# Performance work log

Hardware: AMD Instinct MI355X
Metric: run time of the kernel (lower is better)

The kernel has to match this reference:

```python
import jax, jax.numpy as jnp
import numpy as np

ALPHA = 1.0

def setup_inputs() -> dict:
    key = jax.random.key(0)
    k1, k2, k3, k4 = jax.random.split(key, 4)
    B, N, D = 2048, 32768, 128
    return {
        "anchor": jax.random.normal(k1, (B, D), dtype=jnp.float32),
        "positive": jax.random.normal(k2, (B, D), dtype=jnp.float32),
        "negative": jax.random.normal(k3, (N, D), dtype=jnp.float32),
        "r_score": jax.random.normal(k4, (B, 1), dtype=jnp.float32),
    }

def reference(anchor, positive, negative, r_score):
    # pos_sim: [B,1] elementwise dot per row
    pos_sim = jnp.sum(anchor * positive, axis=1, keepdims=True)
    # neg_mul: [B,N] score matrix; row-wise stable logsumexp -> [B,1]
    neg_mul = jnp.matmul(anchor, negative.T)
    neg_sim = jax.scipy.special.logsumexp(neg_mul, axis=1, keepdims=True)
    loss = jax.nn.relu(neg_sim - pos_sim + r_score + ALPHA)
    return jnp.mean(loss)
```

## Files before the change

kernel.cpp:

```cpp
#include <hip/hip_runtime.h>
#include <hip/hip_bf16.h>


#define B_ROWS 2048
#define N_NEG  32768
#define DIM    128
#define LOG2E  1.4426950408889634f
#define LN2    0.6931471805599453f

typedef __bf16 bf16x8 __attribute__((ext_vector_type(8)));
typedef float  f32x4  __attribute__((ext_vector_type(4)));

static __device__ inline unsigned short f2bf(float f) {
    union { float f; unsigned u; } v; v.f = f;
    unsigned r = v.u + 0x7FFF + ((v.u >> 16) & 1);
    return (unsigned short)(r >> 16);
}

static __device__ inline void load_lds16(const void* g, void* s) {
    __builtin_amdgcn_global_load_lds(
        (const __attribute__((address_space(1))) void*)g,
        (__attribute__((address_space(3))) void*)s,
        16, 0, 0);
}

__global__ void prep(const float* __restrict__ anchor,
                     const float* __restrict__ positive,
                     const float* __restrict__ neg,
                     unsigned short* __restrict__ a_bf,
                     unsigned short* __restrict__ n_bf,
                     float* __restrict__ pos_sim,
                     float* __restrict__ sumexp) {
    int t = threadIdx.x;
    if (blockIdx.x < 256) {
        int row = blockIdx.x * 8 + (t >> 5);
        int c4  = (t & 31) * 4;
        const float4 a4 = *(const float4*)(anchor   + row * DIM + c4);
        const float4 p4 = *(const float4*)(positive + row * DIM + c4);
        float dot = a4.x * p4.x + a4.y * p4.y + a4.z * p4.z + a4.w * p4.w;
        ushort4 ab;
        ab.x = f2bf(a4.x * LOG2E); ab.y = f2bf(a4.y * LOG2E);
        ab.z = f2bf(a4.z * LOG2E); ab.w = f2bf(a4.w * LOG2E);
        *(ushort4*)(a_bf + row * DIM + c4) = ab;
        #pragma unroll
        for (int m = 1; m <= 16; m <<= 1) dot += __shfl_xor(dot, m, 64);
        if ((t & 31) == 0) { pos_sim[row] = dot; sumexp[row] = 0.0f; }
    } else {
        int i = (blockIdx.x - 256) * 256 + t;
        #pragma unroll
        for (int k = 0; k < 4; k++) {
            int idx = i + k * (1024 * 256);
            float4 v = *(const float4*)(neg + (size_t)idx * 4);
            ushort4 o;
            o.x = f2bf(v.x); o.y = f2bf(v.y); o.z = f2bf(v.z); o.w = f2bf(v.w);
            *(ushort4*)(n_bf + (size_t)idx * 4) = o;
        }
    }
}

#define CHUNK 1024
#define TSTEPS (CHUNK / 128)

__global__ __launch_bounds__(256, 2) void fused_gemm_lse(
        const unsigned short* __restrict__ A,
        const unsigned short* __restrict__ Nb,
        float* __restrict__ sumexp) {
    __shared__ unsigned short lds[2][128 * 128];

    const int bid     = blockIdx.x;
    const int rowTile = bid & 15;
    const int chunk   = bid >> 4;
    const int wave = threadIdx.x >> 6, lane = threadIdx.x & 63;
    const int wr = wave >> 1, wc = wave & 1;
    const int q = lane >> 4, c = lane & 15;
    const int lrow = lane >> 4;
    const int lchk = lane & 15;

    const unsigned short* Ag = A + rowTile * (128 * DIM);
    const unsigned short* Bg = Nb + (size_t)(chunk * CHUNK) * DIM;

    #pragma unroll
    for (int i = 0; i < 8; i++) {
        int off = wave * 4096 + i * 512;
        int r   = (off >> 7) + lrow;
        int gofs = r * DIM + ((lchk ^ (r & 7)) << 3);
        load_lds16(Ag + gofs, &lds[0][off]);
        load_lds16(Bg + gofs, &lds[1][off]);
    }
    asm volatile("s_waitcnt vmcnt(0)" ::: "memory");
    __syncthreads();

    int swz[4];
    #pragma unroll
    for (int k = 0; k < 4; k++) swz[k] = (((k * 4 + q) ^ (c & 7)) << 3);

    bf16x8 af[4][4];
    #pragma unroll
    for (int i = 0; i < 4; i++) {
        int row = wr * 64 + i * 16 + c;
        #pragma unroll
        for (int k = 0; k < 4; k++)
            af[i][k] = *(const bf16x8*)&lds[0][row * DIM + swz[k]];
    }
    __syncthreads();

    const f32x4 zero4 = {0.f, 0.f, 0.f, 0.f};
    f32x4 sumacc[4] = {zero4, zero4, zero4, zero4};

    for (int t = 0; t < TSTEPS; t++) {
        const int cur = 1 - (t & 1);
        const int nxt = t & 1;
        if (t + 1 < TSTEPS) {
            const unsigned short* Bn = Bg + (size_t)(t + 1) * 128 * DIM;
            #pragma unroll
            for (int i = 0; i < 8; i++) {
                int off = wave * 4096 + i * 512;
                int r   = (off >> 7) + lrow;
                int gofs = r * DIM + ((lchk ^ (r & 7)) << 3);
                load_lds16(Bn + gofs, &lds[nxt][off]);
            }
        }
        #pragma unroll
        for (int j = 0; j < 4; j++) {
            int brow = wc * 64 + j * 16 + c;
            bf16x8 bf[4];
            #pragma unroll
            for (int k = 0; k < 4; k++)
                bf[k] = *(const bf16x8*)&lds[cur][brow * DIM + swz[k]];
            #pragma unroll
            for (int i = 0; i < 4; i++) {
                f32x4 acc = __builtin_amdgcn_mfma_f32_16x16x32_bf16(af[i][0], bf[0], zero4, 0, 0, 0);
                acc = __builtin_amdgcn_mfma_f32_16x16x32_bf16(af[i][1], bf[1], acc, 0, 0, 0);
                acc = __builtin_amdgcn_mfma_f32_16x16x32_bf16(af[i][2], bf[2], acc, 0, 0, 0);
                acc = __builtin_amdgcn_mfma_f32_16x16x32_bf16(af[i][3], bf[3], acc, 0, 0, 0);
                sumacc[i][0] += __builtin_amdgcn_exp2f(acc[0]);
                sumacc[i][1] += __builtin_amdgcn_exp2f(acc[1]);
                sumacc[i][2] += __builtin_amdgcn_exp2f(acc[2]);
                sumacc[i][3] += __builtin_amdgcn_exp2f(acc[3]);
            }
        }
        if (t + 1 < TSTEPS) {
            asm volatile("s_waitcnt vmcnt(0)" ::: "memory");
            __syncthreads();
        }
    }

    #pragma unroll
    for (int i = 0; i < 4; i++) {
        #pragma unroll
        for (int r = 0; r < 4; r++) {
            float v = sumacc[i][r];
            v += __shfl_xor(v, 1, 64);
            v += __shfl_xor(v, 2, 64);
            v += __shfl_xor(v, 4, 64);
            v += __shfl_xor(v, 8, 64);
            if ((lane & 15) == 0) {
                int row = rowTile * 128 + wr * 64 + i * 16 + q * 4 + r;
                atomicAdd(&sumexp[row], v);
            }
        }
    }
}

__global__ void finalize(const float* __restrict__ sumexp,
                         const float* __restrict__ pos_sim,
                         const float* __restrict__ r_score,
                         float* __restrict__ out) {
    __shared__ float red[4];
    int t = threadIdx.x;
    float acc = 0.0f;
    #pragma unroll
    for (int i = 0; i < 8; i++) {
        int row = t + i * 256;
        float lse  = __log2f(sumexp[row]) * LN2;
        float loss = lse - pos_sim[row] + r_score[row] + 1.0f;
        acc += fmaxf(loss, 0.0f);
    }
    #pragma unroll
    for (int m = 1; m <= 32; m <<= 1) acc += __shfl_xor(acc, m, 64);
    if ((t & 63) == 0) red[t >> 6] = acc;
    __syncthreads();
    if (t == 0) out[0] = (red[0] + red[1] + red[2] + red[3]) * (1.0f / (float)B_ROWS);
}

extern "C" void kernel_launch(void* const* d_in, const int* in_sizes, int n_in,
                              void* d_out, int out_size, void* d_ws, size_t ws_size,
                              hipStream_t stream) {
    const float* anchor   = (const float*)d_in[0];
    const float* positive = (const float*)d_in[1];
    const float* negative = (const float*)d_in[2];
    const float* r_score  = (const float*)d_in[3];
    float* out = (float*)d_out;

    char* ws = (char*)d_ws;
    float* sumexp           = (float*)ws;
    float* pos_sim          = (float*)(ws + 8192);
    unsigned short* a_bf    = (unsigned short*)(ws + 16384);
    unsigned short* n_bf    = (unsigned short*)(ws + 16384 + 524288);

    prep<<<1280, 256, 0, stream>>>(anchor, positive, negative, a_bf, n_bf, pos_sim, sumexp);
    fused_gemm_lse<<<512, 256, 0, stream>>>(a_bf, n_bf, sumexp);
    finalize<<<1, 256, 0, stream>>>(sumexp, pos_sim, r_score, out);
}
```

Baseline: 95.46 us.

## Software-pipeline MFMA with exp2 accumulation and fuse finalize via last-block ticket

```diff
diff --git a/kernel.cpp b/kernel.cpp
--- a/kernel.cpp
+++ b/kernel.cpp
@@ -30,8 +30,10 @@
                      unsigned short* __restrict__ a_bf,
                      unsigned short* __restrict__ n_bf,
                      float* __restrict__ pos_sim,
-                     float* __restrict__ sumexp) {
+                     float* __restrict__ sumexp,
+                     unsigned* __restrict__ counter) {
     int t = threadIdx.x;
+    if (blockIdx.x == 0 && t == 0) counter[0] = 0;
     if (blockIdx.x < 256) {
         int row = blockIdx.x * 8 + (t >> 5);
         int c4  = (t & 31) * 4;
@@ -64,8 +66,14 @@
 __global__ __launch_bounds__(256, 2) void fused_gemm_lse(
         const unsigned short* __restrict__ A,
         const unsigned short* __restrict__ Nb,
-        float* __restrict__ sumexp) {
+        float* __restrict__ sumexp,
+        const float* __restrict__ pos_sim,
+        const float* __restrict__ r_score,
+        unsigned* __restrict__ counter,
+        float* __restrict__ out) {
     __shared__ unsigned short lds[2][128 * 128];
+    __shared__ unsigned lastTicket;
+    __shared__ float red[4];
 
     const int bid     = blockIdx.x;
     const int rowTile = bid & 15;
@@ -106,6 +114,43 @@
 
     const f32x4 zero4 = {0.f, 0.f, 0.f, 0.f};
     f32x4 sumacc[4] = {zero4, zero4, zero4, zero4};
+    const float NINF = -__builtin_huge_valf();
+    const f32x4 ninf4 = {NINF, NINF, NINF, NINF};
+    f32x4 accP[4] = {ninf4, ninf4, ninf4, ninf4};
+    f32x4 accQ[4] = {ninf4, ninf4, ninf4, ninf4};
+
+    bf16x8 bfA[4], bfB[4];
+
+#define STEP(J, BCUR, BNXT, ACCW, ACCE)                                        \
+    {                                                                          \
+        if ((J) < 3) {                                                         \
+            int brow_ = wc * 64 + ((J) + 1) * 16 + c;                          \
+            _Pragma("unroll")                                                  \
+            for (int k = 0; k < 4; k++)                                        \
+                BNXT[k] = *(const bf16x8*)&lds[cur][brow_ * DIM + swz[k]];     \
+        }                                                                      \
+        __builtin_amdgcn_s_setprio(1);                                         \
+        _Pragma("unroll")                                                      \
+        for (int i = 0; i < 4; i++) {                                          \
+            f32x4 a_ = __builtin_amdgcn_mfma_f32_16x16x32_bf16(                \
+                af[i][0], BCUR[0], zero4, 0, 0, 0);                            \
+            a_ = __builtin_amdgcn_mfma_f32_16x16x32_bf16(                      \
+                af[i][1], BCUR[1], a_, 0, 0, 0);                               \
+            a_ = __builtin_amdgcn_mfma_f32_16x16x32_bf16(                      \
+                af[i][2], BCUR[2], a_, 0, 0, 0);                               \
+            a_ = __builtin_amdgcn_mfma_f32_16x16x32_bf16(                      \
+                af[i][3], BCUR[3], a_, 0, 0, 0);                               \
+            ACCW[i] = a_;                                                      \
+        }                                                                      \
+        __builtin_amdgcn_s_setprio(0);                                         \
+        _Pragma("unroll")                                                      \
+        for (int i = 0; i < 4; i++) {                                          \
+            sumacc[i][0] += __builtin_amdgcn_exp2f(ACCE[i][0]);                \
+            sumacc[i][1] += __builtin_amdgcn_exp2f(ACCE[i][1]);                \
+            sumacc[i][2] += __builtin_amdgcn_exp2f(ACCE[i][2]);                \
+            sumacc[i][3] += __builtin_amdgcn_exp2f(ACCE[i][3]);                \
+        }                                                                      \
+    }
 
     for (int t = 0; t < TSTEPS; t++) {
         const int cur = 1 - (t & 1);
@@ -120,29 +165,29 @@
                 load_lds16(Bn + gofs, &lds[nxt][off]);
             }
         }
-        #pragma unroll
-        for (int j = 0; j < 4; j++) {
-            int brow = wc * 64 + j * 16 + c;
-            bf16x8 bf[4];
+        {
+            int brow_ = wc * 64 + c;
             #pragma unroll
             for (int k = 0; k < 4; k++)
-                bf[k] = *(const bf16x8*)&lds[cur][brow * DIM + swz[k]];
-            #pragma unroll
-            for (int i = 0; i < 4; i++) {
-                f32x4 acc = __builtin_amdgcn_mfma_f32_16x16x32_bf16(af[i][0], bf[0], zero4, 0, 0, 0);
-                acc = __builtin_amdgcn_mfma_f32_16x16x32_bf16(af[i][1], bf[1], acc, 0, 0, 0);
-                acc = __builtin_amdgcn_mfma_f32_16x16x32_bf16(af[i][2], bf[2], acc, 0, 0, 0);
-                acc = __builtin_amdgcn_mfma_f32_16x16x32_bf16(af[i][3], bf[3], acc, 0, 0, 0);
-                sumacc[i][0] += __builtin_amdgcn_exp2f(acc[0]);
-                sumacc[i][1] += __builtin_amdgcn_exp2f(acc[1]);
-                sumacc[i][2] += __builtin_amdgcn_exp2f(acc[2]);
-                sumacc[i][3] += __builtin_amdgcn_exp2f(acc[3]);
-            }
-        }
+                bfA[k] = *(const bf16x8*)&lds[cur][brow_ * DIM + swz[k]];
+        }
+        STEP(0, bfA, bfB, accQ, accP)
+        STEP(1, bfB, bfA, accP, accQ)
+        STEP(2, bfA, bfB, accQ, accP)
+        STEP(3, bfB, bfA, accP, accQ)
         if (t + 1 < TSTEPS) {
             asm volatile("s_waitcnt vmcnt(0)" ::: "memory");
             __syncthreads();
         }
+    }
+#undef STEP
+
+    #pragma unroll
+    for (int i = 0; i < 4; i++) {
+        sumacc[i][0] += __builtin_amdgcn_exp2f(accP[i][0]);
+        sumacc[i][1] += __builtin_amdgcn_exp2f(accP[i][1]);
+        sumacc[i][2] += __builtin_amdgcn_exp2f(accP[i][2]);
+        sumacc[i][3] += __builtin_amdgcn_exp2f(accP[i][3]);
     }
 
     #pragma unroll
@@ -160,27 +205,30 @@
             }
         }
     }
-}
-
-__global__ void finalize(const float* __restrict__ sumexp,
-                         const float* __restrict__ pos_sim,
-                         const float* __restrict__ r_score,
-                         float* __restrict__ out) {
-    __shared__ float red[4];
-    int t = threadIdx.x;
-    float acc = 0.0f;
-    #pragma unroll
-    for (int i = 0; i < 8; i++) {
-        int row = t + i * 256;
-        float lse  = __log2f(sumexp[row]) * LN2;
-        float loss = lse - pos_sim[row] + r_score[row] + 1.0f;
-        acc += fmaxf(loss, 0.0f);
-    }
-    #pragma unroll
-    for (int m = 1; m <= 32; m <<= 1) acc += __shfl_xor(acc, m, 64);
-    if ((t & 63) == 0) red[t >> 6] = acc;
-    __syncthreads();
-    if (t == 0) out[0] = (red[0] + red[1] + red[2] + red[3]) * (1.0f / (float)B_ROWS);
+
+    __threadfence();
+    __syncthreads();
+    if (threadIdx.x == 0) lastTicket = atomicAdd(counter, 1u);
+    __syncthreads();
+    if (lastTicket == 511) {
+        int t = threadIdx.x;
+        float acc = 0.0f;
+        #pragma unroll
+        for (int i = 0; i < 8; i++) {
+            int row = t + i * 256;
+            float se = __hip_atomic_load(&sumexp[row], __ATOMIC_RELAXED,
+                                         __HIP_MEMORY_SCOPE_AGENT);
+            float lse  = __log2f(se) * LN2;
+            float loss = lse - pos_sim[row] + r_score[row] + 1.0f;
+            acc += fmaxf(loss, 0.0f);
+        }
+        #pragma unroll
+        for (int m = 1; m <= 32; m <<= 1) acc += __shfl_xor(acc, m, 64);
+        if ((t & 63) == 0) red[t >> 6] = acc;
+        __syncthreads();
+        if (t == 0)
+            out[0] = (red[0] + red[1] + red[2] + red[3]) * (1.0f / (float)B_ROWS);
+    }
 }
 
 extern "C" void kernel_launch(void* const* d_in, const int* in_sizes, int n_in,
@@ -195,10 +243,12 @@
     char* ws = (char*)d_ws;
     float* sumexp           = (float*)ws;
     float* pos_sim          = (float*)(ws + 8192);
-    unsigned short* a_bf    = (unsigned short*)(ws + 16384);
-    unsigned short* n_bf    = (unsigned short*)(ws + 16384 + 524288);
-
-    prep<<<1280, 256, 0, stream>>>(anchor, positive, negative, a_bf, n_bf, pos_sim, sumexp);
-    fused_gemm_lse<<<512, 256, 0, stream>>>(a_bf, n_bf, sumexp);
-    finalize<<<1, 256, 0, stream>>>(sumexp, pos_sim, r_score, out);
-}
+    unsigned* counter       = (unsigned*)(ws + 16384);
+    unsigned short* a_bf    = (unsigned short*)(ws + 20480);
+    unsigned short* n_bf    = (unsigned short*)(ws + 20480 + 524288);
+
+    prep<<<1280, 256, 0, stream>>>(anchor, positive, negative, a_bf, n_bf,
+                                   pos_sim, sumexp, counter);
+    fused_gemm_lse<<<512, 256, 0, stream>>>(a_bf, n_bf, sumexp, pos_sim,
+                                            r_score, counter, out);
+}
```

New measurement: 123.0 us. +28.8%, slower.

## Load negative tiles directly into registers and remap blocks per XCD

Applied to the files above, without the earlier changes.

```diff
diff --git a/kernel.cpp b/kernel.cpp
--- a/kernel.cpp
+++ b/kernel.cpp
@@ -58,18 +58,18 @@
     }
 }
 
-#define CHUNK 1024
-#define TSTEPS (CHUNK / 128)
-
-__global__ __launch_bounds__(256, 2) void fused_gemm_lse(
+__global__ __launch_bounds__(256, 3) void fused_gemm_lse(
         const unsigned short* __restrict__ A,
         const unsigned short* __restrict__ Nb,
         float* __restrict__ sumexp) {
-    __shared__ unsigned short lds[2][128 * 128];
+    __shared__ unsigned short ldsA[128 * 128];
 
-    const int bid     = blockIdx.x;
-    const int rowTile = bid & 15;
-    const int chunk   = bid >> 4;
+    const int bid  = blockIdx.x;
+    const int xcd  = bid & 7;
+    const int slot = bid >> 3;
+    const int rowTile = slot & 15;
+    const int chunk   = xcd * 8 + (slot >> 4);
+
     const int wave = threadIdx.x >> 6, lane = threadIdx.x & 63;
     const int wr = wave >> 1, wc = wave & 1;
     const int q = lane >> 4, c = lane & 15;
@@ -77,15 +77,13 @@
     const int lchk = lane & 15;
 
     const unsigned short* Ag = A + rowTile * (128 * DIM);
-    const unsigned short* Bg = Nb + (size_t)(chunk * CHUNK) * DIM;
 
     #pragma unroll
     for (int i = 0; i < 8; i++) {
         int off = wave * 4096 + i * 512;
         int r   = (off >> 7) + lrow;
         int gofs = r * DIM + ((lchk ^ (r & 7)) << 3);
-        load_lds16(Ag + gofs, &lds[0][off]);
-        load_lds16(Bg + gofs, &lds[1][off]);
+        load_lds16(Ag + gofs, &ldsA[off]);
     }
     asm volatile("s_waitcnt vmcnt(0)" ::: "memory");
     __syncthreads();
@@ -100,48 +98,45 @@
         int row = wr * 64 + i * 16 + c;
         #pragma unroll
         for (int k = 0; k < 4; k++)
-            af[i][k] = *(const bf16x8*)&lds[0][row * DIM + swz[k]];
+            af[i][k] = *(const bf16x8*)&ldsA[row * DIM + swz[k]];
     }
-    __syncthreads();
 
     const f32x4 zero4 = {0.f, 0.f, 0.f, 0.f};
     f32x4 sumacc[4] = {zero4, zero4, zero4, zero4};
 
-    for (int t = 0; t < TSTEPS; t++) {
-        const int cur = 1 - (t & 1);
-        const int nxt = t & 1;
-        if (t + 1 < TSTEPS) {
-            const unsigned short* Bn = Bg + (size_t)(t + 1) * 128 * DIM;
+    const unsigned short* bp =
+        Nb + ((size_t)(chunk * 512 + wc * 256) + c) * DIM + q * 8;
+
+    bf16x8 bf[2][4];
+    #pragma unroll
+    for (int k = 0; k < 4; k++)
+        bf[0][k] = *(const bf16x8*)(bp + k * 32);
+
+    #pragma unroll
+    for (int j = 0; j < 16; j++) {
+        if (j + 1 < 16) {
+            const unsigned short* bn = bp + (j + 1) * (16 * DIM);
             #pragma unroll
-            for (int i = 0; i < 8; i++) {
-                int off = wave * 4096 + i * 512;
-                int r   = (off >> 7) + lrow;
-                int gofs = r * DIM + ((lchk ^ (r & 7)) << 3);
-                load_lds16(Bn + gofs, &lds[nxt][off]);
-            }
+            for (int k = 0; k < 4; k++)
+                bf[(j + 1) & 1][k] = *(const bf16x8*)(bn + k * 32);
+        }
+        f32x4 acc0 = __builtin_amdgcn_mfma_f32_16x16x32_bf16(af[0][0], bf[j & 1][0], zero4, 0, 0, 0);
+        f32x4 acc1 = __builtin_amdgcn_mfma_f32_16x16x32_bf16(af[1][0], bf[j & 1][0], zero4, 0, 0, 0);
+        f32x4 acc2 = __builtin_amdgcn_mfma_f32_16x16x32_bf16(af[2][0], bf[j & 1][0], zero4, 0, 0, 0);
+        f32x4 acc3 = __builtin_amdgcn_mfma_f32_16x16x32_bf16(af[3][0], bf[j & 1][0], zero4, 0, 0, 0);
+        #pragma unroll
+        for (int k = 1; k < 4; k++) {
+            acc0 = __builtin_amdgcn_mfma_f32_16x16x32_bf16(af[0][k], bf[j & 1][k], acc0, 0, 0, 0);
+            acc1 = __builtin_amdgcn_mfma_f32_16x16x32_bf16(af[1][k], bf[j & 1][k], acc1, 0, 0, 0);
+            acc2 = __builtin_amdgcn_mfma_f32_16x16x32_bf16(af[2][k], bf[j & 1][k], acc2, 0, 0, 0);
+            acc3 = __builtin_amdgcn_mfma_f32_16x16x32_bf16(af[3][k], bf[j & 1][k], acc3, 0, 0, 0);
         }
         #pragma unroll
-        for (int j = 0; j < 4; j++) {
-            int brow = wc * 64 + j * 16 + c;
-            bf16x8 bf[4];
-            #pragma unroll
-            for (int k = 0; k < 4; k++)
-                bf[k] = *(const bf16x8*)&lds[cur][brow * DIM + swz[k]];
-            #pragma unroll
-            for (int i = 0; i < 4; i++) {
-                f32x4 acc = __builtin_amdgcn_mfma_f32_16x16x32_bf16(af[i][0], bf[0], zero4, 0, 0, 0);
-                acc = __builtin_amdgcn_mfma_f32_16x16x32_bf16(af[i][1], bf[1], acc, 0, 0, 0);
-                acc = __builtin_amdgcn_mfma_f32_16x16x32_bf16(af[i][2], bf[2], acc, 0, 0, 0);
-                acc = __builtin_amdgcn_mfma_f32_16x16x32_bf16(af[i][3], bf[3], acc, 0, 0, 0);
-                sumacc[i][0] += __builtin_amdgcn_exp2f(acc[0]);
-                sumacc[i][1] += __builtin_amdgcn_exp2f(acc[1]);
-                sumacc[i][2] += __builtin_amdgcn_exp2f(acc[2]);
-                sumacc[i][3] += __builtin_amdgcn_exp2f(acc[3]);
-            }
-        }
-        if (t + 1 < TSTEPS) {
-            asm volatile("s_waitcnt vmcnt(0)" ::: "memory");
-            __syncthreads();
+        for (int r = 0; r < 4; r++) {
+            sumacc[0][r] += __builtin_amdgcn_exp2f(acc0[r]);
+            sumacc[1][r] += __builtin_amdgcn_exp2f(acc1[r]);
+            sumacc[2][r] += __builtin_amdgcn_exp2f(acc2[r]);
+            sumacc[3][r] += __builtin_amdgcn_exp2f(acc3[r]);
         }
     }
 
@@ -199,6 +194,6 @@
     unsigned short* n_bf    = (unsigned short*)(ws + 16384 + 524288);
 
     prep<<<1280, 256, 0, stream>>>(anchor, positive, negative, a_bf, n_bf, pos_sim, sumexp);
-    fused_gemm_lse<<<512, 256, 0, stream>>>(a_bf, n_bf, sumexp);
+    fused_gemm_lse<<<1024, 256, 0, stream>>>(a_bf, n_bf, sumexp);
     finalize<<<1, 256, 0, stream>>>(sumexp, pos_sim, r_score, out);
 }
```

After: 297.0 us. 211% more time.

## Halve LDS footprint with 64-row B tiles and remap blocks across XCDs

Applied to the files above, without the earlier changes.

```diff
diff --git a/kernel.cpp b/kernel.cpp
--- a/kernel.cpp
+++ b/kernel.cpp
@@ -58,18 +58,21 @@
     }
 }
 
-#define CHUNK 1024
-#define TSTEPS (CHUNK / 128)
-
-__global__ __launch_bounds__(256, 2) void fused_gemm_lse(
+#define CHUNK 512
+#define TSTEPS (CHUNK / 64)
+
+__global__ __launch_bounds__(256, 4) void fused_gemm_lse(
         const unsigned short* __restrict__ A,
         const unsigned short* __restrict__ Nb,
         float* __restrict__ sumexp) {
-    __shared__ unsigned short lds[2][128 * 128];
-
-    const int bid     = blockIdx.x;
-    const int rowTile = bid & 15;
-    const int chunk   = bid >> 4;
+    __shared__ unsigned short lds[16384];
+
+    const int bid  = blockIdx.x;
+    const int xcd  = bid & 7;
+    const int slot = bid >> 3;
+    const int rowTile = slot & 15;
+    const int chunk   = xcd * 8 + (slot >> 4);
+
     const int wave = threadIdx.x >> 6, lane = threadIdx.x & 63;
     const int wr = wave >> 1, wc = wave & 1;
     const int q = lane >> 4, c = lane & 15;
@@ -84,8 +87,7 @@
         int off = wave * 4096 + i * 512;
         int r   = (off >> 7) + lrow;
         int gofs = r * DIM + ((lchk ^ (r & 7)) << 3);
-        load_lds16(Ag + gofs, &lds[0][off]);
-        load_lds16(Bg + gofs, &lds[1][off]);
+        load_lds16(Ag + gofs, &lds[off]);
     }
     asm volatile("s_waitcnt vmcnt(0)" ::: "memory");
     __syncthreads();
@@ -100,33 +102,43 @@
         int row = wr * 64 + i * 16 + c;
         #pragma unroll
         for (int k = 0; k < 4; k++)
-            af[i][k] = *(const bf16x8*)&lds[0][row * DIM + swz[k]];
-    }
+            af[i][k] = *(const bf16x8*)&lds[row * DIM + swz[k]];
+    }
+    __syncthreads();
+
+    #pragma unroll
+    for (int i = 0; i < 4; i++) {
+        int off = wave * 2048 + i * 512;
+        int r   = (off >> 7) + lrow;
+        int gofs = r * DIM + ((lchk ^ (r & 7)) << 3);
+        load_lds16(Bg + gofs, &lds[off]);
+    }
+    asm volatile("s_waitcnt vmcnt(0)" ::: "memory");
     __syncthreads();
 
     const f32x4 zero4 = {0.f, 0.f, 0.f, 0.f};
     f32x4 sumacc[4] = {zero4, zero4, zero4, zero4};
 
     for (int t = 0; t < TSTEPS; t++) {
-        const int cur = 1 - (t & 1);
-        const int nxt = t & 1;
+        const int curb = (t & 1) * 8192;
+        const int nxtb = 8192 - curb;
         if (t + 1 < TSTEPS) {
-            const unsigned short* Bn = Bg + (size_t)(t + 1) * 128 * DIM;
+            const unsigned short* Bn = Bg + (size_t)(t + 1) * 64 * DIM;
             #pragma unroll
-            for (int i = 0; i < 8; i++) {
-                int off = wave * 4096 + i * 512;
+            for (int i = 0; i < 4; i++) {
+                int off = wave * 2048 + i * 512;
                 int r   = (off >> 7) + lrow;
                 int gofs = r * DIM + ((lchk ^ (r & 7)) << 3);
-                load_lds16(Bn + gofs, &lds[nxt][off]);
+                load_lds16(Bn + gofs, &lds[nxtb + off]);
             }
         }
         #pragma unroll
-        for (int j = 0; j < 4; j++) {
-            int brow = wc * 64 + j * 16 + c;
+        for (int j = 0; j < 2; j++) {
+            int brow = wc * 32 + j * 16 + c;
             bf16x8 bf[4];
             #pragma unroll
             for (int k = 0; k < 4; k++)
-                bf[k] = *(const bf16x8*)&lds[cur][brow * DIM + swz[k]];
+                bf[k] = *(const bf16x8*)&lds[curb + brow * DIM + swz[k]];
             #pragma unroll
             for (int i = 0; i < 4; i++) {
                 f32x4 acc = __builtin_amdgcn_mfma_f32_16x16x32_bf16(af[i][0], bf[0], zero4, 0, 0, 0);
@@ -199,6 +211,6 @@
     unsigned short* n_bf    = (unsigned short*)(ws + 16384 + 524288);
 
     prep<<<1280, 256, 0, stream>>>(anchor, positive, negative, a_bf, n_bf, pos_sim, sumexp);
-    fused_gemm_lse<<<512, 256, 0, stream>>>(a_bf, n_bf, sumexp);
+    fused_gemm_lse<<<1024, 256, 0, stream>>>(a_bf, n_bf, sumexp);
     finalize<<<1, 256, 0, stream>>>(sumexp, pos_sim, r_score, out);
 }
```

Result: slower. 161.1 us (+68.8%).
